# Kernel tuning notes

Measured on AMD Instinct MI355X. Metric: run time of the kernel, lower is better.

The kernel has to match this reference:

```python
import jax, jax.numpy as jnp
import numpy as np

D_MODEL = 1024
N_HEADS = 16
D_HEAD = D_MODEL // N_HEADS
WINDOW = 256
DILATION = 1
GLOBAL_IDX = (0,)
NEG_INF = float('-inf')


def longformer_mask(seq_len):
    # Vectorized version of the original O(S^2) Python-loop mask builder.
    i = jnp.arange(seq_len)[:, None]
    j = jnp.arange(seq_len)[None, :]
    d = jnp.abs(i - j)
    window_ok = (d <= WINDOW) & (d % DILATION == 0)  # includes diagonal (d==0)
    is_global = jnp.zeros((seq_len,), dtype=bool).at[jnp.array(GLOBAL_IDX)].set(True)
    global_ok = is_global[:, None] | is_global[None, :]
    return jnp.where(window_ok | global_ok, 0.0, NEG_INF).astype(jnp.float32)


def setup_inputs() -> dict:
    key = jax.random.key(0)
    ks = jax.random.split(key, 9)
    s = 1.0 / np.sqrt(D_MODEL)
    inp = {'x': jax.random.normal(ks[0], (2, 2048, D_MODEL), dtype=jnp.float32)}
    for n, kw, kb in (('q', ks[1], ks[2]), ('k', ks[3], ks[4]), ('v', ks[5], ks[6]), ('o', ks[7], ks[8])):
        inp['W' + n] = jax.random.uniform(kw, (D_MODEL, D_MODEL), jnp.float32, -s, s)
        inp['b' + n] = jax.random.uniform(kb, (D_MODEL,), jnp.float32, -s, s)
    return inp


def reference(x, Wq, bq, Wk, bk, Wv, bv, Wo, bo):
    B, S, _ = x.shape
    scale = D_HEAD ** -0.5

    def split_heads(t):  # [B,S,D] -> [B,H,S,d]
        return t.reshape(B, S, N_HEADS, D_HEAD).transpose(0, 2, 1, 3)

    Q = split_heads(x @ Wq + bq)
    K = split_heads(x @ Wk + bk)
    V = split_heads(x @ Wv + bv)

    scores = jnp.einsum('bhqd,bhkd->bhqk', Q, K) * scale
    scores = scores + longformer_mask(S)[None, None]
    attn = jax.nn.softmax(scores, axis=-1)  # dropout is identity in eval
    out = jnp.einsum('bhqk,bhkd->bhqd', attn, V)
    out = out.transpose(0, 2, 1, 3).reshape(B, S, D_MODEL)
    return out @ Wo + bo
```

## Files before the change

### kernel.cpp

```cpp
#include <hip/hip_runtime.h>
#include <hip/hip_bf16.h>

typedef __attribute__((ext_vector_type(8))) short short8;
typedef __attribute__((ext_vector_type(4))) float floatx4;
typedef __attribute__((ext_vector_type(8))) _Float16 half8;
typedef __attribute__((ext_vector_type(4))) _Float16 half4;

using bf16 = __hip_bfloat16;
using fp16 = _Float16;

#define S_LEN 2048
#define DM 1024
#define NH 16
#define DH 64
#define WIN 256

__device__ __forceinline__ unsigned short f2b(float f) {
  __hip_bfloat16 h = __float2bfloat16(f);
  return *reinterpret_cast<unsigned short*>(&h);
}
__device__ __forceinline__ unsigned short f2h(float f) {
  fp16 h = (fp16)f;
  return *reinterpret_cast<unsigned short*>(&h);
}
__device__ __forceinline__ void lds_load16(void* lds, const void* gptr) {
  __builtin_amdgcn_global_load_lds(
      (const __attribute__((address_space(1))) unsigned int*)gptr,
      (__attribute__((address_space(3))) unsigned int*)lds, 16, 0, 0);
}

__global__ __launch_bounds__(256) void k_prep(const float* __restrict__ x,
                                              const float* __restrict__ W0,
                                              const float* __restrict__ W1,
                                              const float* __restrict__ W2,
                                              const float* __restrict__ W3,
                                              bf16* __restrict__ wT,
                                              ushort4* __restrict__ xb) {
  const int tx = threadIdx.x, ty = threadIdx.y;
  if (blockIdx.z == 4) {
    const int tid = ty * 32 + tx;
    const int blk = blockIdx.y * 32 + blockIdx.x;
    const float4* in4 = (const float4*)x;
    #pragma unroll
    for (int k = 0; k < 4; ++k) {
      int i = k * 262144 + blk * 256 + tid;
      float4 v = in4[i];
      ushort4 o;
      o.x = f2b(v.x); o.y = f2b(v.y); o.z = f2b(v.z); o.w = f2b(v.w);
      xb[i] = o;
    }
    return;
  }
  __shared__ float t[32][33];
  const float* W = (blockIdx.z == 0) ? W0 : (blockIdx.z == 1) ? W1 : (blockIdx.z == 2) ? W2 : W3;
  bf16* O = wT + (size_t)blockIdx.z * 1024 * 1024;
  int x0 = blockIdx.x * 32, y0 = blockIdx.y * 32;
  #pragma unroll
  for (int i = 0; i < 32; i += 8) t[ty + i][tx] = W[(size_t)(y0 + ty + i) * 1024 + x0 + tx];
  __syncthreads();
  #pragma unroll
  for (int i = 0; i < 32; i += 8)
    O[(size_t)(x0 + ty + i) * 1024 + y0 + tx] = __float2bfloat16(t[tx][ty + i]);
}

template <int MODE>
__global__ __launch_bounds__(256) void k_gemm(const bf16* __restrict__ A,
                                              const bf16* __restrict__ Bt,
                                              const float* __restrict__ bias_q,
                                              const float* __restrict__ bias_k,
                                              const float* __restrict__ bias_v,
                                              fp16* __restrict__ Qh, fp16* __restrict__ Kh,
                                              fp16* __restrict__ Vt, float* __restrict__ outF) {
  __shared__ __align__(16) bf16 As[2][128 * 32];
  __shared__ __align__(16) bf16 Bs[2][128 * 32];
  const int tid = threadIdx.x;
  const int wave = tid >> 6, lane = tid & 63;
  const int gi = blockIdx.x;
  const int xcd = gi & 7, grr = gi >> 3;
  const int m0 = (xcd * 4 + (grr & 3)) * 128;
  const int n0 = (grr >> 2) * 128;
  const int r0 = tid >> 2;
  const int cb = (tid & 3) * 16;
  const char* Ag = (const char*)A + (size_t)(m0 + r0) * 2048 + cb;
  const char* Bg = (const char*)Bt + (size_t)(n0 + r0) * 2048 + cb;
  char* As0W = (char*)&As[0][0] + wave * 1024;
  char* As1W = (char*)&As[1][0] + wave * 1024;
  char* Bs0W = (char*)&Bs[0][0] + wave * 1024;
  char* Bs1W = (char*)&Bs[1][0] + wave * 1024;
  const int wm = (wave & 1) * 64, wn = (wave >> 1) * 64;
  const int ln = lane & 15, quad = lane >> 4;

  floatx4 acc[4][4];
  #pragma unroll
  for (int i = 0; i < 4; i++)
    #pragma unroll
    for (int j = 0; j < 4; j++) acc[i][j] = (floatx4){0.f, 0.f, 0.f, 0.f};

  for (int k0 = 0; k0 < 1024; k0 += 64) {
    __syncthreads();
    lds_load16(As0W,        Ag + k0 * 2);
    lds_load16(As0W + 4096, Ag + 64 * 2048 + k0 * 2);
    lds_load16(As1W,        Ag + k0 * 2 + 64);
    lds_load16(As1W + 4096, Ag + 64 * 2048 + k0 * 2 + 64);
    lds_load16(Bs0W,        Bg + k0 * 2);
    lds_load16(Bs0W + 4096, Bg + 64 * 2048 + k0 * 2);
    lds_load16(Bs1W,        Bg + k0 * 2 + 64);
    lds_load16(Bs1W + 4096, Bg + 64 * 2048 + k0 * 2 + 64);
    __syncthreads();
    short8 af0[4], af1[4], bf0[4], bf1[4];
    #pragma unroll
    for (int mi = 0; mi < 4; mi++) {
      af0[mi] = *(const short8*)&As[0][(wm + mi * 16 + ln) * 32 + quad * 8];
      af1[mi] = *(const short8*)&As[1][(wm + mi * 16 + ln) * 32 + quad * 8];
    }
    #pragma unroll
    for (int ni = 0; ni < 4; ni++) {
      bf0[ni] = *(const short8*)&Bs[0][(wn + ni * 16 + ln) * 32 + quad * 8];
      bf1[ni] = *(const short8*)&Bs[1][(wn + ni * 16 + ln) * 32 + quad * 8];
    }
    #pragma unroll
    for (int mi = 0; mi < 4; mi++)
      #pragma unroll
      for (int ni = 0; ni < 4; ni++) {
        acc[mi][ni] = __builtin_amdgcn_mfma_f32_16x16x32_bf16(af0[mi], bf0[ni], acc[mi][ni], 0, 0, 0);
        acc[mi][ni] = __builtin_amdgcn_mfma_f32_16x16x32_bf16(af1[mi], bf1[ni], acc[mi][ni], 0, 0, 0);
      }
  }

  if constexpr (MODE == 0) {
    #pragma unroll
    for (int ni = 0; ni < 4; ni++) {
      int n = n0 + wn + ni * 16 + ln;
      int g = n >> 10, nn = n & 1023;
      int h = nn >> 6, dd = nn & 63;
      if (g == 2) {
        float bias = bias_v[nn];
        #pragma unroll
        for (int mi = 0; mi < 4; mi++) {
          int m = m0 + wm + mi * 16 + quad * 4;
          int b = m >> 11, s = m & 2047;
          ushort4 pk;
          pk.x = f2h(acc[mi][ni][0] + bias);
          pk.y = f2h(acc[mi][ni][1] + bias);
          pk.z = f2h(acc[mi][ni][2] + bias);
          pk.w = f2h(acc[mi][ni][3] + bias);
          *(ushort4*)&Vt[((size_t)(b * NH + h) * DH + dd) * S_LEN + s] = pk;
        }
      } else {
        const float* bp = (g == 0) ? bias_q : bias_k;
        fp16* og = (g == 0) ? Qh : Kh;
        float bias = bp[nn];
        #pragma unroll
        for (int mi = 0; mi < 4; mi++) {
          #pragma unroll
          for (int r = 0; r < 4; r++) {
            int m = m0 + wm + mi * 16 + quad * 4 + r;
            int b = m >> 11, s = m & 2047;
            og[(size_t)((b * NH + h) * S_LEN + s) * DH + dd] = (fp16)(acc[mi][ni][r] + bias);
          }
        }
      }
    }
  } else {
    #pragma unroll
    for (int ni = 0; ni < 4; ni++) {
      int n = n0 + wn + ni * 16 + ln;
      float bias = bias_q[n];
      #pragma unroll
      for (int mi = 0; mi < 4; mi++)
        #pragma unroll
        for (int r = 0; r < 4; r++) {
          int m = m0 + wm + mi * 16 + quad * 4 + r;
          outF[(size_t)m * 1024 + n] = acc[mi][ni][r] + bias;
        }
    }
  }
}

__global__ __launch_bounds__(256, 4) void k_attn(const fp16* __restrict__ Qh,
                                                 const fp16* __restrict__ Kh,
                                                 const fp16* __restrict__ Vt,
                                                 bf16* __restrict__ aout) {
  __shared__ __align__(16) fp16 KsL[2][64 * 72];
  __shared__ __align__(16) fp16 VsL[2][64 * 72];

  const int i = blockIdx.x;
  const int xcd = i & 7, rr = i >> 3;
  const int bh = xcd * 4 + (rr & 3);
  const int tile = rr >> 2;
  const int b = bh >> 4, h = bh & 15;
  const size_t base = (size_t)bh * S_LEN * DH;
  const fp16* Qp = Qh + base;
  const fp16* Kp = Kh + base;
  const fp16* Vp = Vt + base;
  const float SC2 = 0.18033688011112042f;
  const int tid = threadIdx.x;

  if (tile == 32) {
    float* sP = (float*)&KsL[0][0];
    float* oR = (float*)&VsL[0][0];
    float* red = (float*)&VsL[1][0];
    const int wv = tid >> 6, lane = tid & 63;
    const int g = lane >> 3, e8 = lane & 7;
    const half8 q0t = *(const half8*)(Qp + e8 * 8);
    float lsum = 0.f;
    for (int it = 0; it < 64; ++it) {
      int grp = wv * 64 + it;
      const half8 kv = *(const half8*)(Kp + (size_t)(grp * 8 + g) * DH + e8 * 8);
      float p = 0.f;
      #pragma unroll
      for (int e = 0; e < 8; ++e) p += (float)q0t[e] * (float)kv[e];
      p += __shfl_xor(p, 1, 64);
      p += __shfl_xor(p, 2, 64);
      p += __shfl_xor(p, 4, 64);
      p = exp2f(fmaf(p, SC2, -8.f));
      if (e8 == 0) sP[grp * 8 + g] = p;
      lsum += p;
    }
    #pragma unroll
    for (int off = 1; off < 64; off <<= 1) lsum += __shfl_xor(lsum, off, 64);
    if (lane == 0) red[wv] = lsum;
    __syncthreads();
    const float ltot = (red[0] + red[1] + red[2] + red[3]) * 0.125f;
    const int d = tid & 63, qu = tid >> 6;
    float o = 0.f;
    for (int j0 = qu * 512; j0 < qu * 512 + 512; j0 += 8) {
      half8 vv = *(const half8*)(Vp + (size_t)d * S_LEN + j0);
      #pragma unroll
      for (int e = 0; e < 8; ++e) o += sP[j0 + e] * (float)vv[e];
    }
    oR[tid] = o;
    __syncthreads();
    if (tid < 64) {
      float oo = oR[tid] + oR[tid + 64] + oR[tid + 128] + oR[tid + 192];
      aout[(size_t)(b * S_LEN) * DM + h * DH + tid] = __float2bfloat16(oo / ltot);
    }
    return;
  }

  const int w = tid >> 6, lane = tid & 63;
  const int ln = lane & 15, quad = lane >> 4;
  const int qb = tile * 64;
  const int qw = qb + w * 16;

  const half8 bq0 = *(const half8*)(Qp + (size_t)(qw + ln) * DH + quad * 8);
  const half8 bq1 = *(const half8*)(Qp + (size_t)(qw + ln) * DH + 32 + quad * 8);

  floatx4 acc[4];
  float l_i;

  {
    const half8 k0a = *(const half8*)(Kp + quad * 8);
    const half8 k0b = *(const half8*)(Kp + 32 + quad * 8);
    float s0 = 0.f;
    #pragma unroll
    for (int e = 0; e < 8; ++e)
      s0 += (float)bq0[e] * (float)k0a[e] + (float)bq1[e] * (float)k0b[e];
    s0 += __shfl_xor(s0, 16, 64);
    s0 += __shfl_xor(s0, 32, 64);
    float p0 = exp2f(fmaf(s0, SC2, -8.f));
    l_i = (quad == 0) ? p0 : 0.f;
    #pragma unroll
    for (int dt = 0; dt < 4; ++dt)
      #pragma unroll
      for (int r = 0; r < 4; ++r)
        acc[dt][r] = p0 * (float)Vp[(size_t)(dt * 16 + quad * 4 + r) * S_LEN];
  }

  int cs = qb - WIN; if (cs < 0) cs = 0;
  int ce = qb + 64 + WIN; if (ce > S_LEN) ce = S_LEN;

  const int f0 = tid, f1 = tid + 256;
  const int r0s = f0 >> 3, c0s = (f0 & 7) * 8;
  const int r1s = f1 >> 3, c1s = (f1 & 7) * 8;

  uint4 kreg0, kreg1, vreg0, vreg1;
  auto stage_load = [&](int c) {
    kreg0 = *(const uint4*)(Kp + (size_t)(c + r0s) * DH + c0s);
    kreg1 = *(const uint4*)(Kp + (size_t)(c + r1s) * DH + c1s);
    vreg0 = *(const uint4*)(Vp + (size_t)r0s * S_LEN + c + c0s);
    vreg1 = *(const uint4*)(Vp + (size_t)r1s * S_LEN + c + c1s);
  };
  auto stage_write = [&](int buf) {
    *(uint4*)&KsL[buf][r0s * 72 + c0s] = kreg0;
    *(uint4*)&KsL[buf][r1s * 72 + c1s] = kreg1;
    *(uint4*)&VsL[buf][r0s * 72 + c0s] = vreg0;
    *(uint4*)&VsL[buf][r1s * 72 + c1s] = vreg1;
  };

  auto compute = [&](int c, int buf) {
    floatx4 s[4];
    #pragma unroll
    for (int jt = 0; jt < 4; ++jt) {
      half8 k0 = *(const half8*)&KsL[buf][(jt * 16 + ln) * 72 + quad * 8];
      half8 k1 = *(const half8*)&KsL[buf][(jt * 16 + ln) * 72 + 32 + quad * 8];
      floatx4 z = (floatx4){0.f, 0.f, 0.f, 0.f};
      z = __builtin_amdgcn_mfma_f32_16x16x32_f16(k0, bq0, z, 0, 0, 0);
      s[jt] = __builtin_amdgcn_mfma_f32_16x16x32_f16(k1, bq1, z, 0, 0, 0);
    }
    half4 v01[8];
    #pragma unroll
    for (int dt = 0; dt < 2; ++dt)
      #pragma unroll
      for (int jt = 0; jt < 4; ++jt)
        v01[dt * 4 + jt] =
            *(const half4*)&VsL[buf][(dt * 16 + ln) * 72 + jt * 16 + quad * 4];
    const bool full_in = (c != 0) && (c >= qw - 241) && (c <= qw + 193);
    half4 Pt[4];
    if (full_in) {
      #pragma unroll
      for (int jt = 0; jt < 4; ++jt)
        #pragma unroll
        for (int r = 0; r < 4; ++r) {
          float pe = exp2f(fmaf(s[jt][r], SC2, -8.f));
          Pt[jt][r] = (fp16)pe;
          l_i += pe;
        }
    } else {
      const int q = qw + ln;
      #pragma unroll
      for (int jt = 0; jt < 4; ++jt) {
        #pragma unroll
        for (int r = 0; r < 4; ++r) {
          int j = c + jt * 16 + quad * 4 + r;
          int dq = q - j;
          bool ok = (dq <= WIN && dq >= -WIN) && (j != 0);
          float pe = ok ? exp2f(fmaf(s[jt][r], SC2, -8.f)) : 0.f;
          Pt[jt][r] = (fp16)pe;
          l_i += pe;
        }
      }
    }
    half4 v23[8];
    #pragma unroll
    for (int dt = 0; dt < 2; ++dt)
      #pragma unroll
      for (int jt = 0; jt < 4; ++jt)
        v23[dt * 4 + jt] =
            *(const half4*)&VsL[buf][((dt + 2) * 16 + ln) * 72 + jt * 16 + quad * 4];
    #pragma unroll
    for (int jt = 0; jt < 4; ++jt) {
      acc[0] = __builtin_amdgcn_mfma_f32_16x16x16f16(v01[jt], Pt[jt], acc[0], 0, 0, 0);
      acc[1] = __builtin_amdgcn_mfma_f32_16x16x16f16(v01[4 + jt], Pt[jt], acc[1], 0, 0, 0);
    }
    #pragma unroll
    for (int jt = 0; jt < 4; ++jt) {
      acc[2] = __builtin_amdgcn_mfma_f32_16x16x16f16(v23[jt], Pt[jt], acc[2], 0, 0, 0);
      acc[3] = __builtin_amdgcn_mfma_f32_16x16x16f16(v23[4 + jt], Pt[jt], acc[3], 0, 0, 0);
    }
  };

  stage_load(cs);
  stage_write(0);
  __syncthreads();
  int buf = 0;
  for (int c = cs; c < ce; c += 64) {
    const bool hasnext = (c + 64 < ce);
    if (hasnext) stage_load(c + 64);
    compute(c, buf);
    if (hasnext) stage_write(buf ^ 1);
    __syncthreads();
    buf ^= 1;
  }

  float lt = l_i;
  lt += __shfl_xor(lt, 16, 64);
  lt += __shfl_xor(lt, 32, 64);
  const float inv = 1.0f / lt;
  const int q = qw + ln;
  if (q != 0) {
    #pragma unroll
    for (int dt = 0; dt < 4; ++dt) {
      ushort4 pk;
      pk.x = f2b(acc[dt][0] * inv);
      pk.y = f2b(acc[dt][1] * inv);
      pk.z = f2b(acc[dt][2] * inv);
      pk.w = f2b(acc[dt][3] * inv);
      *(ushort4*)&aout[(size_t)(b * S_LEN + q) * DM + h * DH + dt * 16 + quad * 4] = pk;
    }
  }
}

extern "C" void kernel_launch(void* const* d_in, const int* in_sizes, int n_in,
                              void* d_out, int out_size, void* d_ws, size_t ws_size,
                              hipStream_t stream) {
  const float* x  = (const float*)d_in[0];
  const float* Wq = (const float*)d_in[1];
  const float* bq = (const float*)d_in[2];
  const float* Wk = (const float*)d_in[3];
  const float* bk = (const float*)d_in[4];
  const float* Wv = (const float*)d_in[5];
  const float* bv = (const float*)d_in[6];
  const float* Wo = (const float*)d_in[7];
  const float* bo = (const float*)d_in[8];
  float* out = (float*)d_out;

  const size_t SEG = (size_t)4096 * 1024;
  bf16* xb = (bf16*)d_ws;
  bf16* wT = xb + SEG;
  fp16* Qh = (fp16*)(wT + SEG);
  fp16* Kh = Qh + SEG;
  fp16* Vt = Kh + SEG;
  bf16* ao = (bf16*)(Vt + SEG);

  k_prep<<<dim3(32, 32, 5), dim3(32, 8), 0, stream>>>(x, Wq, Wk, Wv, Wo, wT, (ushort4*)xb);
  k_gemm<0><<<dim3(768), dim3(256), 0, stream>>>(xb, wT, bq, bk, bv, Qh, Kh, Vt, nullptr);
  k_attn<<<dim3(1056), dim3(256), 0, stream>>>(Qh, Kh, Vt, ao);
  k_gemm<1><<<dim3(256), dim3(256), 0, stream>>>(ao, wT + (size_t)3 * 1024 * 1024, bo,
                                                 nullptr, nullptr, nullptr, nullptr, nullptr, out);
}
```

Measured before the change: 192.0 us.

## Add dedicated 256x256-tile QKV GEMM kernel with 8-wave ping-pong pipeline

```diff
diff --git a/kernel.cpp b/kernel.cpp
--- a/kernel.cpp
+++ b/kernel.cpp
@@ -61,6 +61,190 @@
   #pragma unroll
   for (int i = 0; i < 32; i += 8)
     O[(size_t)(x0 + ty + i) * 1024 + y0 + tx] = __float2bfloat16(t[tx][ty + i]);
+}
+
+__global__ __launch_bounds__(512) void k_qkv(const bf16* __restrict__ A,
+                                             const bf16* __restrict__ Bt,
+                                             const float* __restrict__ bias_q,
+                                             const float* __restrict__ bias_k,
+                                             const float* __restrict__ bias_v,
+                                             fp16* __restrict__ Qh, fp16* __restrict__ Kh,
+                                             fp16* __restrict__ Vt) {
+  __shared__ __align__(16) char lds[131072];
+  const int tid = threadIdx.x;
+  const int wave = tid >> 6, lane = tid & 63;
+  const int ln = lane & 15, quad = lane >> 4;
+  const int wr = wave >> 2, wc = wave & 3;
+
+  const int gi = blockIdx.x;
+  const int wg = (gi & 7) * 24 + (gi >> 3);
+  const int mt = wg / 12, nt = wg % 12;
+
+  auto mkF = [](int p) {
+    int q = p ^ (((p >> 9) & 1) << 5);
+    int sub = q >> 10;
+    int w = q & 1023;
+    return (((sub >> 1) << 4) + (w >> 6)) * 2048 + (sub & 1) * 64 + (w & 63);
+  };
+  const int F0 = mkF(tid * 16);
+  const int F1 = mkF(8192 + tid * 16);
+  const char* Ab = (const char*)A + (size_t)mt * 524288;
+  const char* Bb = (const char*)Bt + (size_t)nt * 524288;
+
+  auto stg = [&](int region, const char* g) {
+    lds_load16(lds + region + wave * 1024, g + F0);
+    lds_load16(lds + region + 8192 + wave * 1024, g + F1);
+  };
+
+  stg(0, Ab);
+  stg(16384, Ab + 262144);
+  stg(32768, Bb);
+  stg(49152, Bb + 262144);
+  stg(65536, Ab + 128);
+  stg(65536 + 16384, Ab + 262144 + 128);
+  stg(65536 + 32768, Bb + 128);
+  stg(65536 + 49152, Bb + 262144 + 128);
+
+  floatx4 acc[8][4];
+  #pragma unroll
+  for (int i = 0; i < 8; ++i)
+    #pragma unroll
+    for (int j = 0; j < 4; ++j) acc[i][j] = (floatx4){0.f, 0.f, 0.f, 0.f};
+
+  const int lnq = ln * 64 + ((quad * 16) ^ ((ln & 8) << 2));
+  const int aoff = wr * 16384 + lnq;
+  const int boff = 32768 + (wc >> 1) * 16384 + (wc & 1) * 8192 + lnq;
+
+  asm volatile("s_waitcnt vmcnt(8)" ::: "memory");
+  __builtin_amdgcn_s_barrier();
+
+  for (int t = 0; t < 16; ++t) {
+    const char* bb = lds + ((t & 1) << 16);
+    const int sreg = (t & 1) << 16;
+    const char* gA = Ab + (t + 2) * 128;
+    const char* gB = Bb + (t + 2) * 128;
+    const bool pf = (t + 2 < 16);
+
+    short8 a0[4][2], b0[4][2];
+    #pragma unroll
+    for (int m2 = 0; m2 < 4; ++m2)
+      #pragma unroll
+      for (int kk = 0; kk < 2; ++kk)
+        a0[m2][kk] = *(const short8*)(bb + aoff + m2 * 2048 + kk * 1024);
+    #pragma unroll
+    for (int n2 = 0; n2 < 2; ++n2)
+      #pragma unroll
+      for (int kk = 0; kk < 2; ++kk)
+        b0[n2][kk] = *(const short8*)(bb + boff + n2 * 2048 + kk * 1024);
+    __builtin_amdgcn_s_barrier();
+    __builtin_amdgcn_s_setprio(1);
+    #pragma unroll
+    for (int m2 = 0; m2 < 4; ++m2)
+      #pragma unroll
+      for (int n2 = 0; n2 < 2; ++n2) {
+        acc[m2][n2] = __builtin_amdgcn_mfma_f32_16x16x32_bf16(a0[m2][0], b0[n2][0], acc[m2][n2], 0, 0, 0);
+        acc[m2][n2] = __builtin_amdgcn_mfma_f32_16x16x32_bf16(a0[m2][1], b0[n2][1], acc[m2][n2], 0, 0, 0);
+      }
+    __builtin_amdgcn_s_setprio(0);
+    __builtin_amdgcn_s_barrier();
+
+    #pragma unroll
+    for (int n2 = 2; n2 < 4; ++n2)
+      #pragma unroll
+      for (int kk = 0; kk < 2; ++kk)
+        b0[n2][kk] = *(const short8*)(bb + boff + n2 * 2048 + kk * 1024);
+    __builtin_amdgcn_s_barrier();
+    __builtin_amdgcn_s_setprio(1);
+    #pragma unroll
+    for (int m2 = 0; m2 < 4; ++m2)
+      #pragma unroll
+      for (int n2 = 2; n2 < 4; ++n2) {
+        acc[m2][n2] = __builtin_amdgcn_mfma_f32_16x16x32_bf16(a0[m2][0], b0[n2][0], acc[m2][n2], 0, 0, 0);
+        acc[m2][n2] = __builtin_amdgcn_mfma_f32_16x16x32_bf16(a0[m2][1], b0[n2][1], acc[m2][n2], 0, 0, 0);
+      }
+    __builtin_amdgcn_s_setprio(0);
+    __builtin_amdgcn_s_barrier();
+
+    short8 a1[4][2];
+    #pragma unroll
+    for (int m2 = 0; m2 < 4; ++m2)
+      #pragma unroll
+      for (int kk = 0; kk < 2; ++kk)
+        a1[m2][kk] = *(const short8*)(bb + aoff + (4 + m2) * 2048 + kk * 1024);
+    if (pf) {
+      stg(sreg + 32768, gB);
+      stg(sreg + 49152, gB + 262144);
+    }
+    __builtin_amdgcn_s_barrier();
+    __builtin_amdgcn_s_setprio(1);
+    #pragma unroll
+    for (int m2 = 0; m2 < 4; ++m2)
+      #pragma unroll
+      for (int n2 = 0; n2 < 2; ++n2) {
+        acc[4 + m2][n2] = __builtin_amdgcn_mfma_f32_16x16x32_bf16(a1[m2][0], b0[n2][0], acc[4 + m2][n2], 0, 0, 0);
+        acc[4 + m2][n2] = __builtin_amdgcn_mfma_f32_16x16x32_bf16(a1[m2][1], b0[n2][1], acc[4 + m2][n2], 0, 0, 0);
+      }
+    __builtin_amdgcn_s_setprio(0);
+    __builtin_amdgcn_s_barrier();
+
+    if (pf) {
+      stg(sreg, gA);
+      stg(sreg + 16384, gA + 262144);
+      asm volatile("s_waitcnt vmcnt(8)" ::: "memory");
+    } else {
+      asm volatile("s_waitcnt vmcnt(0)" ::: "memory");
+    }
+    __builtin_amdgcn_s_barrier();
+    __builtin_amdgcn_s_setprio(1);
+    #pragma unroll
+    for (int m2 = 0; m2 < 4; ++m2)
+      #pragma unroll
+      for (int n2 = 2; n2 < 4; ++n2) {
+        acc[4 + m2][n2] = __builtin_amdgcn_mfma_f32_16x16x32_bf16(a1[m2][0], b0[n2][0], acc[4 + m2][n2], 0, 0, 0);
+        acc[4 + m2][n2] = __builtin_amdgcn_mfma_f32_16x16x32_bf16(a1[m2][1], b0[n2][1], acc[4 + m2][n2], 0, 0, 0);
+      }
+    __builtin_amdgcn_s_setprio(0);
+    __builtin_amdgcn_s_barrier();
+  }
+
+  const int g = nt >> 2;
+  if (g == 2) {
+    #pragma unroll
+    for (int ni = 0; ni < 4; ++ni) {
+      int nn = (nt & 3) * 256 + wc * 64 + ni * 16 + ln;
+      int h = nn >> 6, dd = nn & 63;
+      float bias = bias_v[nn];
+      #pragma unroll
+      for (int mi = 0; mi < 8; ++mi) {
+        int m = mt * 256 + wr * 128 + mi * 16 + quad * 4;
+        int b = m >> 11, s = m & 2047;
+        ushort4 pk;
+        pk.x = f2h(acc[mi][ni][0] + bias);
+        pk.y = f2h(acc[mi][ni][1] + bias);
+        pk.z = f2h(acc[mi][ni][2] + bias);
+        pk.w = f2h(acc[mi][ni][3] + bias);
+        *(ushort4*)&Vt[((size_t)((b * NH + h) * DH + dd)) * S_LEN + s] = pk;
+      }
+    }
+  } else {
+    const float* bp = (g == 0) ? bias_q : bias_k;
+    fp16* og = (g == 0) ? Qh : Kh;
+    #pragma unroll
+    for (int ni = 0; ni < 4; ++ni) {
+      int nn = (nt & 3) * 256 + wc * 64 + ni * 16 + ln;
+      int h = nn >> 6, dd = nn & 63;
+      float bias = bp[nn];
+      #pragma unroll
+      for (int mi = 0; mi < 8; ++mi) {
+        #pragma unroll
+        for (int r = 0; r < 4; ++r) {
+          int m = mt * 256 + wr * 128 + mi * 16 + quad * 4 + r;
+          int b = m >> 11, s = m & 2047;
+          og[(size_t)((b * NH + h) * S_LEN + s) * DH + dd] = (fp16)(acc[mi][ni][r] + bias);
+        }
+      }
+    }
+  }
 }
 
 template <int MODE>
@@ -404,7 +588,7 @@
   bf16* ao = (bf16*)(Vt + SEG);
 
   k_prep<<<dim3(32, 32, 5), dim3(32, 8), 0, stream>>>(x, Wq, Wk, Wv, Wo, wT, (ushort4*)xb);
-  k_gemm<0><<<dim3(768), dim3(256), 0, stream>>>(xb, wT, bq, bk, bv, Qh, Kh, Vt, nullptr);
+  k_qkv<<<dim3(192), dim3(512), 0, stream>>>(xb, wT, bq, bk, bv, Qh, Kh, Vt);
   k_attn<<<dim3(1056), dim3(256), 0, stream>>>(Qh, Kh, Vt, ao);
   k_gemm<1><<<dim3(256), dim3(256), 0, stream>>>(ao, wT + (size_t)3 * 1024 * 1024, bo,
                                                  nullptr, nullptr, nullptr, nullptr, nullptr, out);
```

New measurement: 190.3 us. About the same (-0.9%).
